# Performance work log

Measured on AMD Instinct MI355X. Metric: run time of the kernel, lower is better.

The kernel has to match this reference:

```python
import jax, jax.numpy as jnp
import numpy as np

N_CELLS = 19683   # 27**3 lattice
K = 26            # Moore-neighborhood max_neighbors
D = 128           # state_size
HG = 64           # gating hidden
CNF_STEPS = 3     # integration_steps
DT = 0.1


def setup_inputs() -> dict:
    key = jax.random.key(0)
    ks = jax.random.split(key, 12)
    s = lambda fan_in: 1.0 / np.sqrt(fan_in)
    return {
        "current_state": jax.random.normal(ks[0], (N_CELLS, D), jnp.float32),
        "neighbor_states": jax.random.normal(ks[1], (N_CELLS, K, D), jnp.float32),
        "conn_type": jax.random.randint(ks[2], (N_CELLS, K), 0, 3, jnp.int32),
        "W_local": jax.random.normal(ks[3], (2 * D, D), jnp.float32) * s(2 * D),
        "b_local": jnp.zeros((D,), jnp.float32),
        "W_msg": jax.random.normal(ks[4], (2 * D, D), jnp.float32) * s(2 * D),
        "b_msg": jnp.zeros((D,), jnp.float32),
        "W_upd": jax.random.normal(ks[5], (2 * D, D), jnp.float32) * s(2 * D),
        "b_upd": jnp.zeros((D,), jnp.float32),
        "W_cnf": jax.random.normal(ks[6], (2 * D, D), jnp.float32) * s(2 * D),
        "b_cnf": jnp.zeros((D,), jnp.float32),
        "W_g1": jax.random.normal(ks[7], (D, HG), jnp.float32) * s(D),
        "b_g1": jnp.zeros((HG,), jnp.float32),
        "W_g2": jax.random.normal(ks[8], (HG, 3), jnp.float32) * s(HG),
        "b_g2": jnp.zeros((3,), jnp.float32),
    }


def _masked_mean(nbr, mask):
    # nbr: [N,K,D], mask: [N,K] float -> [N,D]
    cnt = jnp.maximum(mask.sum(-1, keepdims=True), 1.0)
    return jnp.einsum("nkd,nk->nd", nbr, mask) / cnt


def reference(current_state, neighbor_states, conn_type,
              W_local, b_local, W_msg, b_msg, W_upd, b_upd,
              W_cnf, b_cnf, W_g1, b_g1, W_g2, b_g2):
    cur = current_state                       # [N,D]
    nbr = neighbor_states                     # [N,K,D]
    m_l = (conn_type == 0).astype(cur.dtype)  # local mask   [N,K]
    m_f = (conn_type == 1).astype(cur.dtype)  # functional
    m_d = (conn_type == 2).astype(cur.dtype)  # distant

    # --- local expert: SimpleLinear over [cell, mean(local neighbors)] ---
    agg_l = _masked_mean(nbr, m_l)
    local_out = jnp.tanh(jnp.concatenate([cur, agg_l], -1) @ W_local + b_local)

    # --- functional expert: GNN message passing ---
    cur_b = jnp.broadcast_to(cur[:, None, :], nbr.shape)          # [N,K,D]
    edge_in = jnp.concatenate([cur_b, nbr], -1)                   # [N,K,2D]
    msgs = jax.nn.relu(edge_in @ W_msg + b_msg)                   # [N,K,D]
    agg_msg = _masked_mean(msgs, m_f)                             # [N,D]
    func_out = jnp.tanh(jnp.concatenate([cur, agg_msg], -1) @ W_upd + b_upd)

    # --- distant expert: lightweight CNF (fixed-step Euler) ---
    agg_d = _masked_mean(nbr, m_d)

    def euler_step(s, _):
        ds = jnp.tanh(jnp.concatenate([s, agg_d], -1) @ W_cnf + b_cnf)
        return s + DT * ds, None

    distant_out, _ = jax.lax.scan(euler_step, cur, None, length=CNF_STEPS)

    # --- gating network: softmax over 3 experts ---
    gates = jax.nn.softmax(jax.nn.relu(cur @ W_g1 + b_g1) @ W_g2 + b_g2, -1)  # [N,3]

    out = (gates[:, 0:1] * local_out
           + gates[:, 1:2] * func_out
           + gates[:, 2:3] * distant_out)
    return out
```

## Files before the change

### kernel.cpp

```cpp
#include <hip/hip_runtime.h>
#include <hip/hip_bf16.h>
#include <math.h>

#define NC 19683
#define KN 26
#define DD 128
#define HGN 64
#define LDSB 136
#define DTC 0.1f

using bf8v = __attribute__((ext_vector_type(8))) short;
using f4v  = __attribute__((ext_vector_type(4))) float;

__device__ __forceinline__ unsigned short f2bf(float x) {
    union { float f; unsigned u; } v; v.f = x;
    unsigned r = v.u + 0x7fffu + ((v.u >> 16) & 1u);
    return (unsigned short)(r >> 16);
}
__device__ __forceinline__ unsigned pk2(float a, float b) {
    return ((unsigned)f2bf(a)) | (((unsigned)f2bf(b)) << 16);
}

__global__ __launch_bounds__(256) void k_prep(const float* __restrict__ Wl,
    const float* __restrict__ Wm, const float* __restrict__ Wu,
    const float* __restrict__ Wc, const float* __restrict__ Wg1,
    unsigned short* __restrict__ WT, unsigned short* __restrict__ WgT)
{
    int idx = blockIdx.x * 256 + threadIdx.x;
    if (idx < 131072) {
        int m = idx >> 15;
        int r = idx & 32767;
        int j = r >> 8;
        int i = r & 255;
        const float* src = (m == 0) ? Wl : (m == 1) ? Wm : (m == 2) ? Wu : Wc;
        WT[idx] = f2bf(src[i * DD + j]);
    } else {
        int idx2 = idx - 131072;
        int col = idx2 >> 7;
        int k = idx2 & 127;
        WgT[idx2] = f2bf(Wg1[k * HGN + col]);
    }
}

__global__ __launch_bounds__(256) void kA(const float* __restrict__ cur,
    const unsigned short* __restrict__ WT, const unsigned short* __restrict__ WgT,
    const float* __restrict__ b_msg, const float* __restrict__ bg1,
    const float* __restrict__ Wg2, const float* __restrict__ bg2,
    float* __restrict__ P, float* __restrict__ gates)
{
    __shared__ __align__(16) unsigned short Al[32][LDSB];
    __shared__ __align__(16) unsigned short Bl[128][LDSB];
    __shared__ __align__(16) unsigned short Gl[64][LDSB];
    __shared__ float hrelu[32][HGN + 4];
    int t = threadIdx.x;
    int n0 = blockIdx.x * 32;
    int w = t >> 6, lane = t & 63;
    int lm = lane & 15, lq = lane >> 4;

    for (int p = 0; p < 8; ++p) {
        int idx = p * 256 + t;
        int r = idx >> 6, c2 = (idx & 63) * 2;
        float2 v = {0.f, 0.f};
        if (n0 + r < NC) v = *(const float2*)&cur[(size_t)(n0 + r) * DD + c2];
        *(unsigned*)&Al[r][c2] = pk2(v.x, v.y);
    }
    const unsigned short* WmT = WT + 32768;
    for (int p = 0; p < 8; ++p) {
        int ch = p * 256 + t;
        int j = ch >> 4, i8 = (ch & 15) * 8;
        *(bf8v*)&Bl[j][i8] = *(const bf8v*)&WmT[j * 256 + i8];
    }
    for (int p = 0; p < 4; ++p) {
        int ch = p * 256 + t;
        int j = ch >> 4, i8 = (ch & 15) * 8;
        *(bf8v*)&Gl[j][i8] = *(const bf8v*)&WgT[j * 128 + i8];
    }
    __syncthreads();

    {
        int mt = w & 1, colh = w >> 1;
        for (int nt = 0; nt < 4; ++nt) {
            int col0 = colh * 64 + nt * 16;
            f4v acc = {0.f, 0.f, 0.f, 0.f};
            for (int s = 0; s < 4; ++s) {
                bf8v a = *(const bf8v*)&Al[mt * 16 + lm][s * 32 + lq * 8];
                bf8v b = *(const bf8v*)&Bl[col0 + lm][s * 32 + lq * 8];
                acc = __builtin_amdgcn_mfma_f32_16x16x32_bf16(a, b, acc, 0, 0, 0);
            }
            int col = col0 + lm;
            float bm = b_msg[col];
            for (int r = 0; r < 4; ++r) {
                int row = mt * 16 + lq * 4 + r;
                int n = n0 + row;
                if (n < NC) P[(size_t)n * DD + col] = acc[r] + bm;
            }
        }
    }
    {
        int col0 = w * 16;
        float bg = bg1[col0 + lm];
        for (int mt2 = 0; mt2 < 2; ++mt2) {
            f4v acc = {0.f, 0.f, 0.f, 0.f};
            for (int s = 0; s < 4; ++s) {
                bf8v a = *(const bf8v*)&Al[mt2 * 16 + lm][s * 32 + lq * 8];
                bf8v b = *(const bf8v*)&Gl[col0 + lm][s * 32 + lq * 8];
                acc = __builtin_amdgcn_mfma_f32_16x16x32_bf16(a, b, acc, 0, 0, 0);
            }
            for (int r = 0; r < 4; ++r)
                hrelu[mt2 * 16 + lq * 4 + r][col0 + lm] = fmaxf(acc[r] + bg, 0.f);
        }
    }
    __syncthreads();
    if (t < 32) {
        int n = n0 + t;
        if (n < NC) {
            float l[3];
            for (int e = 0; e < 3; ++e) {
                float s = bg2[e];
                for (int g = 0; g < HGN; ++g) s += hrelu[t][g] * Wg2[g * 3 + e];
                l[e] = s;
            }
            float m = fmaxf(l[0], fmaxf(l[1], l[2]));
            float e0 = expf(l[0] - m), e1 = expf(l[1] - m), e2 = expf(l[2] - m);
            float inv = 1.f / (e0 + e1 + e2);
            gates[n * 4 + 0] = e0 * inv;
            gates[n * 4 + 1] = e1 * inv;
            gates[n * 4 + 2] = e2 * inv;
        }
    }
}

__global__ __launch_bounds__(256) void kB(const float* __restrict__ nbr,
    const int* __restrict__ conn, const unsigned short* __restrict__ WT,
    const float* __restrict__ P, unsigned short* __restrict__ agg_l,
    unsigned short* __restrict__ agg_m, unsigned short* __restrict__ agg_d)
{
    __shared__ __align__(16) unsigned short Bl[128][LDSB];
    __shared__ __align__(16) unsigned short Al[4][32][LDSB];
    __shared__ float P8[4][DD];
    int t = threadIdx.x;
    int n0 = blockIdx.x * 4;
    int w = t >> 6, lane = t & 63;
    int n = n0 + w;
    bool act = n < NC;

    const unsigned short* Wm2T = WT + 32768 + 128;
    for (int p = 0; p < 8; ++p) {
        int ch = p * 256 + t;
        int j = ch >> 4, i8 = (ch & 15) * 8;
        *(bf8v*)&Bl[j][i8] = *(const bf8v*)&Wm2T[j * 256 + i8];
    }
    {
        int idx = t * 2;
        int r = idx >> 7, c = idx & 127;
        float2 v = {0.f, 0.f};
        if (n0 + r < NC) v = *(const float2*)&P[(size_t)(n0 + r) * DD + c];
        *(float2*)&P8[r][c] = v;
    }
    int ct = 3;
    if (act && lane < KN) ct = conn[(size_t)n * KN + lane];
    unsigned long long mlb = __ballot(ct == 0);
    unsigned long long mfb = __ballot(ct == 1);
    unsigned long long mdb = __ballot(ct == 2);
    float icl = 1.f / fmaxf((float)__builtin_popcountll(mlb), 1.f);
    float icf = 1.f / fmaxf((float)__builtin_popcountll(mfb), 1.f);
    float icd = 1.f / fmaxf((float)__builtin_popcountll(mdb), 1.f);

    int j2 = lane * 2;
    const float* base = nbr + ((size_t)(act ? n : 0) * KN) * DD + j2;
    float2 vv[KN];
    #pragma unroll
    for (int k = 0; k < KN; ++k) {
        float2 v = {0.f, 0.f};
        if (act) v = *(const float2*)&base[(size_t)k * DD];
        vv[k] = v;
    }
    float slx = 0.f, sly = 0.f, sdx = 0.f, sdy = 0.f;
    #pragma unroll
    for (int k = 0; k < KN; ++k) {
        float2 v = vv[k];
        if ((mlb >> k) & 1) { slx += v.x; sly += v.y; }
        if ((mdb >> k) & 1) { sdx += v.x; sdy += v.y; }
        *(unsigned*)&Al[w][k][j2] = pk2(v.x, v.y);
    }
    {
        unsigned* pz = (unsigned*)&Al[w][KN][0];
        for (int z = lane; z < (32 - KN) * LDSB / 2; z += 64) pz[z] = 0;
    }
    if (act) {
        *(unsigned*)&agg_l[(size_t)n * DD + j2] = pk2(slx * icl, sly * icl);
        *(unsigned*)&agg_d[(size_t)n * DD + j2] = pk2(sdx * icd, sdy * icd);
    }
    __syncthreads();

    if (act) {
        int lm = lane & 15, lq = lane >> 4;
        for (int nt = 0; nt < 8; ++nt) {
            int col0 = nt * 16;
            float pv = P8[w][col0 + lm];
            float msum = 0.f;
            for (int mt2 = 0; mt2 < 2; ++mt2) {
                f4v acc = {0.f, 0.f, 0.f, 0.f};
                for (int s = 0; s < 4; ++s) {
                    bf8v a = *(const bf8v*)&Al[w][mt2 * 16 + lm][s * 32 + lq * 8];
                    bf8v b = *(const bf8v*)&Bl[col0 + lm][s * 32 + lq * 8];
                    acc = __builtin_amdgcn_mfma_f32_16x16x32_bf16(a, b, acc, 0, 0, 0);
                }
                for (int r = 0; r < 4; ++r) {
                    int row = mt2 * 16 + lq * 4 + r;
                    if ((mfb >> row) & 1) msum += fmaxf(pv + acc[r], 0.f);
                }
            }
            msum += __shfl_xor(msum, 16, 64);
            msum += __shfl_xor(msum, 32, 64);
            if (lane < 16) agg_m[(size_t)n * DD + col0 + lane] = f2bf(msum * icf);
        }
    }
}

__global__ __launch_bounds__(256) void kC(const float* __restrict__ cur,
    const unsigned short* __restrict__ WT, const unsigned short* __restrict__ agg_l,
    const unsigned short* __restrict__ agg_m, const unsigned short* __restrict__ agg_d,
    const float* __restrict__ b_local, const float* __restrict__ b_upd,
    const float* __restrict__ b_cnf, const float* __restrict__ gates,
    float* __restrict__ out)
{
    __shared__ __align__(16) unsigned short Wl[128][LDSB];
    __shared__ __align__(16) unsigned short Xc[32][LDSB];
    __shared__ __align__(16) unsigned short Xa[32][LDSB];
    __shared__ float glds[32][4];
    __shared__ float bl[DD], bu[DD], bc[DD];
    int t = threadIdx.x;
    int n0 = blockIdx.x * 32;
    int w = t >> 6, lane = t & 63;
    int mt = w & 1, colh = w >> 1;
    int lm = lane & 15, lq = lane >> 4;

    auto stageW = [&](int m, int koff) {
        const unsigned short* src = WT + m * 32768 + koff;
        for (int p = 0; p < 8; ++p) {
            int ch = p * 256 + t;
            int j = ch >> 4, i8 = (ch & 15) * 8;
            *(bf8v*)&Wl[j][i8] = *(const bf8v*)&src[j * 256 + i8];
        }
    };
    auto stageXa = [&](const unsigned short* src) {
        for (int p = 0; p < 2; ++p) {
            int idx = p * 256 + t;
            int r = idx >> 4, c8 = (idx & 15) * 8;
            bf8v v = {0, 0, 0, 0, 0, 0, 0, 0};
            if (n0 + r < NC) v = *(const bf8v*)&src[(size_t)(n0 + r) * DD + c8];
            *(bf8v*)&Xa[r][c8] = v;
        }
    };
    auto mfmaPass = [&](unsigned short (&X)[32][LDSB], f4v* acc) {
        for (int nt = 0; nt < 4; ++nt) {
            int col0 = colh * 64 + nt * 16;
            for (int s = 0; s < 4; ++s) {
                bf8v a = *(const bf8v*)&X[mt * 16 + lm][s * 32 + lq * 8];
                bf8v b = *(const bf8v*)&Wl[col0 + lm][s * 32 + lq * 8];
                acc[nt] = __builtin_amdgcn_mfma_f32_16x16x32_bf16(a, b, acc[nt], 0, 0, 0);
            }
        }
    };

    for (int p = 0; p < 8; ++p) {
        int idx = p * 256 + t;
        int r = idx >> 6, c2 = (idx & 63) * 2;
        float2 v = {0.f, 0.f};
        if (n0 + r < NC) v = *(const float2*)&cur[(size_t)(n0 + r) * DD + c2];
        *(unsigned*)&Xc[r][c2] = pk2(v.x, v.y);
    }
    if (t < 128) { bl[t] = b_local[t]; bu[t] = b_upd[t]; bc[t] = b_cnf[t]; }
    if (t >= 128 && t < 160) {
        int r = t - 128; int n = n0 + r;
        float g0 = 0.f, g1 = 0.f, g2 = 0.f;
        if (n < NC) { g0 = gates[n * 4]; g1 = gates[n * 4 + 1]; g2 = gates[n * 4 + 2]; }
        glds[r][0] = g0; glds[r][1] = g1; glds[r][2] = g2;
    }
    stageW(0, 0);
    __syncthreads();

    f4v oacc[4], acc[4];
    for (int nt = 0; nt < 4; ++nt) oacc[nt] = (f4v){0.f, 0.f, 0.f, 0.f};

    for (int nt = 0; nt < 4; ++nt) acc[nt] = (f4v){0.f, 0.f, 0.f, 0.f};
    mfmaPass(Xc, acc);
    __syncthreads();
    stageW(0, 128); stageXa(agg_l);
    __syncthreads();
    mfmaPass(Xa, acc);
    for (int nt = 0; nt < 4; ++nt) {
        int col = colh * 64 + nt * 16 + lm;
        for (int r = 0; r < 4; ++r) {
            int row = mt * 16 + lq * 4 + r;
            oacc[nt][r] += glds[row][0] * tanhf(acc[nt][r] + bl[col]);
        }
    }

    __syncthreads();
    stageW(2, 0);
    __syncthreads();
    for (int nt = 0; nt < 4; ++nt) acc[nt] = (f4v){0.f, 0.f, 0.f, 0.f};
    mfmaPass(Xc, acc);
    __syncthreads();
    stageW(2, 128); stageXa(agg_m);
    __syncthreads();
    mfmaPass(Xa, acc);
    for (int nt = 0; nt < 4; ++nt) {
        int col = colh * 64 + nt * 16 + lm;
        for (int r = 0; r < 4; ++r) {
            int row = mt * 16 + lq * 4 + r;
            oacc[nt][r] += glds[row][1] * tanhf(acc[nt][r] + bu[col]);
        }
    }

    __syncthreads();
    stageW(3, 128); stageXa(agg_d);
    __syncthreads();
    for (int nt = 0; nt < 4; ++nt) acc[nt] = (f4v){0.f, 0.f, 0.f, 0.f};
    mfmaPass(Xa, acc);
    f4v hd[4], s[4];
    for (int nt = 0; nt < 4; ++nt) {
        int col = colh * 64 + nt * 16 + lm;
        for (int r = 0; r < 4; ++r) {
            int row = mt * 16 + lq * 4 + r;
            int n = n0 + row;
            hd[nt][r] = acc[nt][r] + bc[col];
            s[nt][r] = (n < NC) ? cur[(size_t)n * DD + col] : 0.f;
        }
    }
    __syncthreads();
    stageW(3, 0);
    for (int step = 0; step < 3; ++step) {
        for (int nt = 0; nt < 4; ++nt) {
            int col = colh * 64 + nt * 16 + lm;
            for (int r = 0; r < 4; ++r) {
                int row = mt * 16 + lq * 4 + r;
                Xa[row][col] = f2bf(s[nt][r]);
            }
        }
        __syncthreads();
        for (int nt = 0; nt < 4; ++nt) acc[nt] = (f4v){0.f, 0.f, 0.f, 0.f};
        mfmaPass(Xa, acc);
        for (int nt = 0; nt < 4; ++nt)
            for (int r = 0; r < 4; ++r)
                s[nt][r] += DTC * tanhf(acc[nt][r] + hd[nt][r]);
        __syncthreads();
    }

    for (int nt = 0; nt < 4; ++nt) {
        int col = colh * 64 + nt * 16 + lm;
        for (int r = 0; r < 4; ++r) {
            int row = mt * 16 + lq * 4 + r;
            int n = n0 + row;
            if (n < NC) out[(size_t)n * DD + col] = oacc[nt][r] + glds[row][2] * s[nt][r];
        }
    }
}

extern "C" void kernel_launch(void* const* d_in, const int* in_sizes, int n_in,
                              void* d_out, int out_size, void* d_ws, size_t ws_size,
                              hipStream_t stream) {
    const float* cur     = (const float*)d_in[0];
    const float* nbr     = (const float*)d_in[1];
    const int*   conn    = (const int*)d_in[2];
    const float* W_local = (const float*)d_in[3];
    const float* b_local = (const float*)d_in[4];
    const float* W_msg   = (const float*)d_in[5];
    const float* b_msg   = (const float*)d_in[6];
    const float* W_upd   = (const float*)d_in[7];
    const float* b_upd   = (const float*)d_in[8];
    const float* W_cnf   = (const float*)d_in[9];
    const float* b_cnf   = (const float*)d_in[10];
    const float* Wg1     = (const float*)d_in[11];
    const float* bg1     = (const float*)d_in[12];
    const float* Wg2     = (const float*)d_in[13];
    const float* bg2     = (const float*)d_in[14];
    float* out = (float*)d_out;

    char* ws = (char*)d_ws;
    unsigned short* WT  = (unsigned short*)ws;
    unsigned short* WgT = (unsigned short*)(ws + 262144);
    float* P      = (float*)(ws + 278528);
    float* gatesb = (float*)(ws + 278528 + 10077696);
    unsigned short* aggl = (unsigned short*)(ws + 278528 + 10077696 + 314928);
    unsigned short* aggm = aggl + (size_t)NC * DD;
    unsigned short* aggd = aggm + (size_t)NC * DD;

    hipLaunchKernelGGL(k_prep, dim3(544), dim3(256), 0, stream, W_local, W_msg, W_upd, W_cnf, Wg1, WT, WgT);
    hipLaunchKernelGGL(kA, dim3(616), dim3(256), 0, stream, cur, WT, WgT, b_msg, bg1, Wg2, bg2, P, gatesb);
    hipLaunchKernelGGL(kB, dim3(4921), dim3(256), 0, stream, nbr, conn, WT, P, aggl, aggm, aggd);
    hipLaunchKernelGGL(kC, dim3(616), dim3(256), 0, stream, cur, WT, aggl, aggm, aggd, b_local, b_upd, b_cnf, gatesb, out);
}
```

Baseline: 458.2 us.

## Fold kA into kB and kC: compute per-cell message projection and gates inline

Removes the separate kA kernel. The cur@W_msg[:128] projection is now computed inside kB for its 4 cells using a padded 16-row MFMA tile. The gating MLP and softmax move into kC, which reuses its LDS weight buffer. This drops the P and gates round trips through global memory and one launch. In exchange, kB does an extra weight staging pass and two more barriers per block, with most of its MFMA tile wasted on padding rows. kB also issues the neighbor loads before the ballots and raises wave priority during its MFMA loop.

Result: slower. 473.4 us (+3.3%).

```diff
diff --git a/kernel.cpp b/kernel.cpp
--- a/kernel.cpp
+++ b/kernel.cpp
@@ -42,98 +42,11 @@
     }
 }
 
-__global__ __launch_bounds__(256) void kA(const float* __restrict__ cur,
-    const unsigned short* __restrict__ WT, const unsigned short* __restrict__ WgT,
-    const float* __restrict__ b_msg, const float* __restrict__ bg1,
-    const float* __restrict__ Wg2, const float* __restrict__ bg2,
-    float* __restrict__ P, float* __restrict__ gates)
-{
-    __shared__ __align__(16) unsigned short Al[32][LDSB];
-    __shared__ __align__(16) unsigned short Bl[128][LDSB];
-    __shared__ __align__(16) unsigned short Gl[64][LDSB];
-    __shared__ float hrelu[32][HGN + 4];
-    int t = threadIdx.x;
-    int n0 = blockIdx.x * 32;
-    int w = t >> 6, lane = t & 63;
-    int lm = lane & 15, lq = lane >> 4;
-
-    for (int p = 0; p < 8; ++p) {
-        int idx = p * 256 + t;
-        int r = idx >> 6, c2 = (idx & 63) * 2;
-        float2 v = {0.f, 0.f};
-        if (n0 + r < NC) v = *(const float2*)&cur[(size_t)(n0 + r) * DD + c2];
-        *(unsigned*)&Al[r][c2] = pk2(v.x, v.y);
-    }
-    const unsigned short* WmT = WT + 32768;
-    for (int p = 0; p < 8; ++p) {
-        int ch = p * 256 + t;
-        int j = ch >> 4, i8 = (ch & 15) * 8;
-        *(bf8v*)&Bl[j][i8] = *(const bf8v*)&WmT[j * 256 + i8];
-    }
-    for (int p = 0; p < 4; ++p) {
-        int ch = p * 256 + t;
-        int j = ch >> 4, i8 = (ch & 15) * 8;
-        *(bf8v*)&Gl[j][i8] = *(const bf8v*)&WgT[j * 128 + i8];
-    }
-    __syncthreads();
-
-    {
-        int mt = w & 1, colh = w >> 1;
-        for (int nt = 0; nt < 4; ++nt) {
-            int col0 = colh * 64 + nt * 16;
-            f4v acc = {0.f, 0.f, 0.f, 0.f};
-            for (int s = 0; s < 4; ++s) {
-                bf8v a = *(const bf8v*)&Al[mt * 16 + lm][s * 32 + lq * 8];
-                bf8v b = *(const bf8v*)&Bl[col0 + lm][s * 32 + lq * 8];
-                acc = __builtin_amdgcn_mfma_f32_16x16x32_bf16(a, b, acc, 0, 0, 0);
-            }
-            int col = col0 + lm;
-            float bm = b_msg[col];
-            for (int r = 0; r < 4; ++r) {
-                int row = mt * 16 + lq * 4 + r;
-                int n = n0 + row;
-                if (n < NC) P[(size_t)n * DD + col] = acc[r] + bm;
-            }
-        }
-    }
-    {
-        int col0 = w * 16;
-        float bg = bg1[col0 + lm];
-        for (int mt2 = 0; mt2 < 2; ++mt2) {
-            f4v acc = {0.f, 0.f, 0.f, 0.f};
-            for (int s = 0; s < 4; ++s) {
-                bf8v a = *(const bf8v*)&Al[mt2 * 16 + lm][s * 32 + lq * 8];
-                bf8v b = *(const bf8v*)&Gl[col0 + lm][s * 32 + lq * 8];
-                acc = __builtin_amdgcn_mfma_f32_16x16x32_bf16(a, b, acc, 0, 0, 0);
-            }
-            for (int r = 0; r < 4; ++r)
-                hrelu[mt2 * 16 + lq * 4 + r][col0 + lm] = fmaxf(acc[r] + bg, 0.f);
-        }
-    }
-    __syncthreads();
-    if (t < 32) {
-        int n = n0 + t;
-        if (n < NC) {
-            float l[3];
-            for (int e = 0; e < 3; ++e) {
-                float s = bg2[e];
-                for (int g = 0; g < HGN; ++g) s += hrelu[t][g] * Wg2[g * 3 + e];
-                l[e] = s;
-            }
-            float m = fmaxf(l[0], fmaxf(l[1], l[2]));
-            float e0 = expf(l[0] - m), e1 = expf(l[1] - m), e2 = expf(l[2] - m);
-            float inv = 1.f / (e0 + e1 + e2);
-            gates[n * 4 + 0] = e0 * inv;
-            gates[n * 4 + 1] = e1 * inv;
-            gates[n * 4 + 2] = e2 * inv;
-        }
-    }
-}
-
-__global__ __launch_bounds__(256) void kB(const float* __restrict__ nbr,
-    const int* __restrict__ conn, const unsigned short* __restrict__ WT,
-    const float* __restrict__ P, unsigned short* __restrict__ agg_l,
-    unsigned short* __restrict__ agg_m, unsigned short* __restrict__ agg_d)
+__global__ __launch_bounds__(256) void kB(const float* __restrict__ cur,
+    const float* __restrict__ nbr, const int* __restrict__ conn,
+    const unsigned short* __restrict__ WT, const float* __restrict__ b_msg,
+    unsigned short* __restrict__ agg_l, unsigned short* __restrict__ agg_m,
+    unsigned short* __restrict__ agg_d)
 {
     __shared__ __align__(16) unsigned short Bl[128][LDSB];
     __shared__ __align__(16) unsigned short Al[4][32][LDSB];
@@ -143,29 +56,10 @@
     int w = t >> 6, lane = t & 63;
     int n = n0 + w;
     bool act = n < NC;
-
-    const unsigned short* Wm2T = WT + 32768 + 128;
-    for (int p = 0; p < 8; ++p) {
-        int ch = p * 256 + t;
-        int j = ch >> 4, i8 = (ch & 15) * 8;
-        *(bf8v*)&Bl[j][i8] = *(const bf8v*)&Wm2T[j * 256 + i8];
-    }
-    {
-        int idx = t * 2;
-        int r = idx >> 7, c = idx & 127;
-        float2 v = {0.f, 0.f};
-        if (n0 + r < NC) v = *(const float2*)&P[(size_t)(n0 + r) * DD + c];
-        *(float2*)&P8[r][c] = v;
-    }
+    int lm = lane & 15, lq = lane >> 4;
+
     int ct = 3;
     if (act && lane < KN) ct = conn[(size_t)n * KN + lane];
-    unsigned long long mlb = __ballot(ct == 0);
-    unsigned long long mfb = __ballot(ct == 1);
-    unsigned long long mdb = __ballot(ct == 2);
-    float icl = 1.f / fmaxf((float)__builtin_popcountll(mlb), 1.f);
-    float icf = 1.f / fmaxf((float)__builtin_popcountll(mfb), 1.f);
-    float icd = 1.f / fmaxf((float)__builtin_popcountll(mdb), 1.f);
-
     int j2 = lane * 2;
     const float* base = nbr + ((size_t)(act ? n : 0) * KN) * DD + j2;
     float2 vv[KN];
@@ -175,6 +69,51 @@
         if (act) v = *(const float2*)&base[(size_t)k * DD];
         vv[k] = v;
     }
+    unsigned long long mlb = __ballot(ct == 0);
+    unsigned long long mfb = __ballot(ct == 1);
+    unsigned long long mdb = __ballot(ct == 2);
+    float icl = 1.f / fmaxf((float)__builtin_popcountll(mlb), 1.f);
+    float icf = 1.f / fmaxf((float)__builtin_popcountll(mfb), 1.f);
+    float icd = 1.f / fmaxf((float)__builtin_popcountll(mdb), 1.f);
+
+    const unsigned short* Wm1T = WT + 32768;
+    for (int p = 0; p < 8; ++p) {
+        int ch = p * 256 + t;
+        int j = ch >> 4, i8 = (ch & 15) * 8;
+        *(bf8v*)&Bl[j][i8] = *(const bf8v*)&Wm1T[j * 256 + i8];
+    }
+    {
+        int r = t >> 6, c2 = (t & 63) * 2;
+        float2 v = {0.f, 0.f};
+        if (n0 + r < NC) v = *(const float2*)&cur[(size_t)(n0 + r) * DD + c2];
+        *(unsigned*)&Al[0][r][c2] = pk2(v.x, v.y);
+        unsigned* pz = (unsigned*)&Al[0][4][0];
+        for (int z = t; z < 12 * LDSB / 2; z += 256) pz[z] = 0;
+    }
+    __syncthreads();
+
+    for (int nt = 0; nt < 2; ++nt) {
+        int col0 = w * 32 + nt * 16;
+        f4v acc = {0.f, 0.f, 0.f, 0.f};
+        for (int s = 0; s < 4; ++s) {
+            bf8v a = *(const bf8v*)&Al[0][lm][s * 32 + lq * 8];
+            bf8v b = *(const bf8v*)&Bl[col0 + lm][s * 32 + lq * 8];
+            acc = __builtin_amdgcn_mfma_f32_16x16x32_bf16(a, b, acc, 0, 0, 0);
+        }
+        if (lq == 0) {
+            int col = col0 + lm;
+            float bm = b_msg[col];
+            for (int r = 0; r < 4; ++r) P8[r][col] = acc[r] + bm;
+        }
+    }
+    __syncthreads();
+
+    const unsigned short* Wm2T = WT + 32768 + 128;
+    for (int p = 0; p < 8; ++p) {
+        int ch = p * 256 + t;
+        int j = ch >> 4, i8 = (ch & 15) * 8;
+        *(bf8v*)&Bl[j][i8] = *(const bf8v*)&Wm2T[j * 256 + i8];
+    }
     float slx = 0.f, sly = 0.f, sdx = 0.f, sdy = 0.f;
     #pragma unroll
     for (int k = 0; k < KN; ++k) {
@@ -194,7 +133,7 @@
     __syncthreads();
 
     if (act) {
-        int lm = lane & 15, lq = lane >> 4;
+        __builtin_amdgcn_s_setprio(1);
         for (int nt = 0; nt < 8; ++nt) {
             int col0 = nt * 16;
             float pv = P8[w][col0 + lm];
@@ -215,21 +154,27 @@
             msum += __shfl_xor(msum, 32, 64);
             if (lane < 16) agg_m[(size_t)n * DD + col0 + lane] = f2bf(msum * icf);
         }
+        __builtin_amdgcn_s_setprio(0);
     }
 }
 
 __global__ __launch_bounds__(256) void kC(const float* __restrict__ cur,
-    const unsigned short* __restrict__ WT, const unsigned short* __restrict__ agg_l,
-    const unsigned short* __restrict__ agg_m, const unsigned short* __restrict__ agg_d,
+    const unsigned short* __restrict__ WT, const unsigned short* __restrict__ WgT,
+    const unsigned short* __restrict__ agg_l, const unsigned short* __restrict__ agg_m,
+    const unsigned short* __restrict__ agg_d,
     const float* __restrict__ b_local, const float* __restrict__ b_upd,
-    const float* __restrict__ b_cnf, const float* __restrict__ gates,
+    const float* __restrict__ b_cnf, const float* __restrict__ bg1,
+    const float* __restrict__ Wg2, const float* __restrict__ bg2,
     float* __restrict__ out)
 {
     __shared__ __align__(16) unsigned short Wl[128][LDSB];
     __shared__ __align__(16) unsigned short Xc[32][LDSB];
     __shared__ __align__(16) unsigned short Xa[32][LDSB];
+    __shared__ float hrelu[32][HGN + 4];
     __shared__ float glds[32][4];
     __shared__ float bl[DD], bu[DD], bc[DD];
+    __shared__ float Wg2s[HGN * 3];
+    __shared__ float bg2s[4];
     int t = threadIdx.x;
     int n0 = blockIdx.x * 32;
     int w = t >> 6, lane = t & 63;
@@ -271,16 +216,48 @@
         if (n0 + r < NC) v = *(const float2*)&cur[(size_t)(n0 + r) * DD + c2];
         *(unsigned*)&Xc[r][c2] = pk2(v.x, v.y);
     }
+    for (int p = 0; p < 4; ++p) {
+        int ch = p * 256 + t;
+        int j = ch >> 4, i8 = (ch & 15) * 8;
+        *(bf8v*)&Wl[j][i8] = *(const bf8v*)&WgT[j * 128 + i8];
+    }
     if (t < 128) { bl[t] = b_local[t]; bu[t] = b_upd[t]; bc[t] = b_cnf[t]; }
-    if (t >= 128 && t < 160) {
-        int r = t - 128; int n = n0 + r;
-        float g0 = 0.f, g1 = 0.f, g2 = 0.f;
-        if (n < NC) { g0 = gates[n * 4]; g1 = gates[n * 4 + 1]; g2 = gates[n * 4 + 2]; }
-        glds[r][0] = g0; glds[r][1] = g1; glds[r][2] = g2;
-    }
+    for (int i = t; i < HGN * 3; i += 256) Wg2s[i] = Wg2[i];
+    if (t < 3) bg2s[t] = bg2[t];
+    __syncthreads();
+
+    {
+        int col0 = w * 16;
+        float bg = bg1[col0 + lm];
+        for (int mt2 = 0; mt2 < 2; ++mt2) {
+            f4v acc = {0.f, 0.f, 0.f, 0.f};
+            for (int s = 0; s < 4; ++s) {
+                bf8v a = *(const bf8v*)&Xc[mt2 * 16 + lm][s * 32 + lq * 8];
+                bf8v b = *(const bf8v*)&Wl[col0 + lm][s * 32 + lq * 8];
+                acc = __builtin_amdgcn_mfma_f32_16x16x32_bf16(a, b, acc, 0, 0, 0);
+            }
+            for (int r = 0; r < 4; ++r)
+                hrelu[mt2 * 16 + lq * 4 + r][col0 + lm] = fmaxf(acc[r] + bg, 0.f);
+        }
+    }
+    __syncthreads();
+
     stageW(0, 0);
-    __syncthreads();
-
+    if (t < 96) {
+        int r = t / 3, e = t - r * 3;
+        float s = bg2s[e];
+        for (int g = 0; g < HGN; ++g) s += hrelu[r][g] * Wg2s[g * 3 + e];
+        glds[r][e] = s;
+    }
+    __syncthreads();
+
+    if (t < 32) {
+        float l0 = glds[t][0], l1 = glds[t][1], l2 = glds[t][2];
+        float m = fmaxf(l0, fmaxf(l1, l2));
+        float e0 = expf(l0 - m), e1 = expf(l1 - m), e2 = expf(l2 - m);
+        float inv = 1.f / (e0 + e1 + e2);
+        glds[t][0] = e0 * inv; glds[t][1] = e1 * inv; glds[t][2] = e2 * inv;
+    }
     f4v oacc[4], acc[4];
     for (int nt = 0; nt < 4; ++nt) oacc[nt] = (f4v){0.f, 0.f, 0.f, 0.f};
 
@@ -380,16 +357,14 @@
     float* out = (float*)d_out;
 
     char* ws = (char*)d_ws;
-    unsigned short* WT  = (unsigned short*)ws;
-    unsigned short* WgT = (unsigned short*)(ws + 262144);
-    float* P      = (float*)(ws + 278528);
-    float* gatesb = (float*)(ws + 278528 + 10077696);
-    unsigned short* aggl = (unsigned short*)(ws + 278528 + 10077696 + 314928);
+    unsigned short* WT   = (unsigned short*)ws;
+    unsigned short* WgT  = (unsigned short*)(ws + 262144);
+    unsigned short* aggl = (unsigned short*)(ws + 278528);
     unsigned short* aggm = aggl + (size_t)NC * DD;
     unsigned short* aggd = aggm + (size_t)NC * DD;
 
     hipLaunchKernelGGL(k_prep, dim3(544), dim3(256), 0, stream, W_local, W_msg, W_upd, W_cnf, Wg1, WT, WgT);
-    hipLaunchKernelGGL(kA, dim3(616), dim3(256), 0, stream, cur, WT, WgT, b_msg, bg1, Wg2, bg2, P, gatesb);
-    hipLaunchKernelGGL(kB, dim3(4921), dim3(256), 0, stream, nbr, conn, WT, P, aggl, aggm, aggd);
-    hipLaunchKernelGGL(kC, dim3(616), dim3(256), 0, stream, cur, WT, aggl, aggm, aggd, b_local, b_upd, b_cnf, gatesb, out);
-}
+    hipLaunchKernelGGL(kB, dim3(4921), dim3(256), 0, stream, cur, nbr, conn, WT, b_msg, aggl, aggm, aggd);
+    hipLaunchKernelGGL(kC, dim3(616), dim3(256), 0, stream, cur, WT, WgT, aggl, aggm, aggd,
+                       b_local, b_upd, b_cnf, bg1, Wg2, bg2, out);
+}
```
